# Performance work log

Measured on AMD Instinct MI355X. Metric: run time of the kernel, lower is better.

Reference implementation:

```python
import jax, jax.numpy as jnp
import numpy as np

NEG = 1e12


def _sincos(seq_len, dim):
    # SinusoidalPositionEmbedding with merge_mode='zero': [1, S, dim] interleaved (sin, cos)
    pos = jnp.arange(seq_len, dtype=jnp.float32)
    inv = jnp.power(10000.0, -2.0 * jnp.arange(dim // 2, dtype=jnp.float32) / dim)
    emb = pos[:, None] * inv[None, :]                      # [S, dim/2]
    emb = jnp.stack([jnp.sin(emb), jnp.cos(emb)], axis=-1).reshape(seq_len, dim)
    cos_pos = jnp.repeat(emb[:, 1::2], 2, axis=-1)[None]   # [1, S, dim]
    sin_pos = jnp.repeat(emb[:, ::2], 2, axis=-1)[None]    # [1, S, dim]
    return cos_pos, sin_pos


def _rope(x, cos_pos, sin_pos):
    # x: [B, S, d]; rotate pairs: (-x1, x0, -x3, x2, ...)
    x2 = jnp.stack([-x[..., 1::2], x[..., ::2]], axis=-1).reshape(x.shape)
    return x * cos_pos + x2 * sin_pos


def _pointer_head(hidden, mask_f, W1, b1, W2, b2, inner_dim):
    B, S, _ = hidden.shape
    out = hidden @ W1 + b1                                 # [B, S, 2*inner_dim]
    qw, kw = out[..., ::2], out[..., 1::2]                 # [B, S, inner_dim]
    cos_pos, sin_pos = _sincos(S, inner_dim)
    qw = _rope(qw, cos_pos, sin_pos)
    kw = _rope(kw, cos_pos, sin_pos)
    logits = jnp.einsum('bmd,bnd->bmn', qw, kw) / (inner_dim ** 0.5)  # [B, S, S]
    bias = jnp.transpose(hidden @ W2 + b2, (0, 2, 1)) / 2.0           # [B, 2T, S]
    # [B, T, S, S]
    logits = logits[:, None] + bias[:, ::2, None, :] + bias[:, 1::2, :, None]
    # sequence masking on key axis (last) and query axis (second-to-last)
    mk = mask_f[:, None, None, :]
    mq = mask_f[:, None, :, None]
    logits = logits * mq - NEG * (1.0 - mq)
    logits = logits * mk - NEG * (1.0 - mk)
    # strict lower-triangular mask over (m, n)
    tril = jnp.tril(jnp.ones((S, S), dtype=logits.dtype), k=-1)
    logits = logits - tril * NEG
    return logits


def setup_inputs() -> dict:
    key = jax.random.key(0)
    ks = jax.random.split(key, 10)
    B, S, H = 8, 512, 768
    inner_dim, ent_t, arg_t = 64, 12, 16
    s = 0.02
    return {
        'last_hidden_state': jax.random.normal(ks[0], (B, S, H), jnp.float32),
        'attention_mask': jnp.ones((B, S), jnp.int32),
        'W1': jax.random.normal(ks[1], (H, inner_dim * 2), jnp.float32) * s,
        'b1': jax.random.normal(ks[2], (inner_dim * 2,), jnp.float32) * s,
        'W2': jax.random.normal(ks[3], (H, ent_t * 2), jnp.float32) * s,
        'b2': jax.random.normal(ks[4], (ent_t * 2,), jnp.float32) * s,
        'Wa1': jax.random.normal(ks[5], (H, inner_dim * 2), jnp.float32) * s,
        'ba1': jax.random.normal(ks[6], (inner_dim * 2,), jnp.float32) * s,
        'Wa2': jax.random.normal(ks[7], (H, arg_t * 2), jnp.float32) * s,
        'ba2': jax.random.normal(ks[8], (arg_t * 2,), jnp.float32) * s,
    }


def reference(last_hidden_state, attention_mask, W1, b1, W2, b2, Wa1, ba1, Wa2, ba2):
    inner_dim = W1.shape[1] // 2
    mask_f = attention_mask.astype(last_hidden_state.dtype)
    logits = _pointer_head(last_hidden_state, mask_f, W1, b1, W2, b2, inner_dim)
    argument_logits = _pointer_head(last_hidden_state, mask_f, Wa1, ba1, Wa2, ba2, inner_dim)
    return logits, argument_logits
```

## Files before the change

### kernel.cpp

```cpp
#include <hip/hip_runtime.h>
#include <hip/hip_bf16.h>

typedef __attribute__((ext_vector_type(8))) short s16x8;
typedef __attribute__((ext_vector_type(4))) float f32x4;

#define NEGC 1000000000000.0f

constexpr int B_ = 8, S_ = 512, H_ = 768;
constexpr int ENT = 12, ARG = 16;
constexpr int NC = 320;
constexpr int ROWS = B_ * S_;
constexpr size_t OUT_ENT = (size_t)B_ * ENT * S_ * S_;

static __device__ __forceinline__ unsigned short f2bf(float x) {
  return __builtin_bit_cast(unsigned short, __float2bfloat16(x));
}

typedef const __attribute__((address_space(1))) unsigned int gu32;
typedef __attribute__((address_space(3))) unsigned int lu32;
static __device__ __forceinline__ void glds16(const void* g, void* l) {
  __builtin_amdgcn_global_load_lds((gu32*)g, (lu32*)l, 16, 0, 0);
}

__global__ __launch_bounds__(256) void k_prep(
    const float* __restrict__ X,
    const float* __restrict__ W1, const float* __restrict__ b1,
    const float* __restrict__ W2, const float* __restrict__ b2,
    const float* __restrict__ Wa1, const float* __restrict__ ba1,
    const float* __restrict__ Wa2, const float* __restrict__ ba2,
    __hip_bfloat16* __restrict__ Xb,
    __hip_bfloat16* __restrict__ Wt,
    float* __restrict__ bcat) {
  int idx = blockIdx.x * 256 + threadIdx.x;
  const int nx = ROWS * H_ / 4;
  if (idx < nx) {
    float4 v = reinterpret_cast<const float4*>(X)[idx];
    ushort4 o;
    o.x = f2bf(v.x); o.y = f2bf(v.y); o.z = f2bf(v.z); o.w = f2bf(v.w);
    reinterpret_cast<ushort4*>(Xb)[idx] = o;
    return;
  }
  idx -= nx;
  if (idx < NC * H_) {
    int n = idx / H_;
    int k = idx - n * H_;
    float v = 0.0f;
    if (n < 128)      v = W1[k * 128 + n];
    else if (n < 152) v = W2[k * 24 + (n - 128)];
    else if (n < 280) v = Wa1[k * 128 + (n - 152)];
    else if (n < 312) v = Wa2[k * 32 + (n - 280)];
    reinterpret_cast<unsigned short*>(Wt)[(size_t)n * H_ + k] = f2bf(v);
    return;
  }
  idx -= NC * H_;
  if (idx < NC) {
    int n = idx;
    float v = 0.0f;
    if (n < 128)      v = b1[n];
    else if (n < 152) v = b2[n - 128];
    else if (n < 280) v = ba1[n - 152];
    else if (n < 312) v = ba2[n - 280];
    bcat[n] = v;
  }
}

__global__ __launch_bounds__(256) void k_gemm(
    const __hip_bfloat16* __restrict__ Xb,
    const __hip_bfloat16* __restrict__ Wt,
    const float* __restrict__ bcat,
    __hip_bfloat16* __restrict__ qwe, __hip_bfloat16* __restrict__ kwe,
    __hip_bfloat16* __restrict__ qwa, __hip_bfloat16* __restrict__ kwa,
    float* __restrict__ kbe, float* __restrict__ qbe,
    float* __restrict__ kba, float* __restrict__ qba) {
  __shared__ __hip_bfloat16 XA[2][32 * 64];
  __shared__ __hip_bfloat16 WA[2][64 * 64];
  const int tid  = threadIdx.x;
  const int lane = tid & 63;
  const int w    = tid >> 6;
  const int wm   = w & 1;
  const int wn   = w >> 1;
  const int rl   = lane & 15;
  const int rg   = lane >> 4;
  const int row0 = blockIdx.y * 32;
  const int col0 = blockIdx.x * 64;
  const int lr = lane >> 3, cc = lane & 7;
  const int scs = cc ^ lr;

  const short* Xs = reinterpret_cast<const short*>(Xb);
  const short* Ws = reinterpret_cast<const short*>(Wt);
  const size_t xsrc  = (size_t)(row0 + w * 8 + lr) * H_ + scs * 8;
  const size_t wsrc0 = (size_t)(col0 + w * 16 + lr) * H_ + scs * 8;
  const size_t wsrc1 = (size_t)(col0 + w * 16 + 8 + lr) * H_ + scs * 8;

  auto stage = [&](int t, int buf) {
    const size_t ko = (size_t)t * 64;
    glds16(Xs + xsrc + ko,  &XA[buf][(w * 8) * 64]);
    glds16(Ws + wsrc0 + ko, &WA[buf][(w * 16) * 64]);
    glds16(Ws + wsrc1 + ko, &WA[buf][(w * 16 + 8) * 64]);
  };

  f32x4 acc[2] = {};
  auto compute = [&](int buf) {
    const short* xl = reinterpret_cast<const short*>(XA[buf]);
    const short* wl = reinterpret_cast<const short*>(WA[buf]);
#pragma unroll
    for (int ks = 0; ks < 2; ++ks) {
      const int gc = ks * 4 + rg;
      const int mloc = wm * 16 + rl;
      s16x8 bfrag = *reinterpret_cast<const s16x8*>(xl + mloc * 64 + (gc ^ (rl & 7)) * 8);
#pragma unroll
      for (int ni = 0; ni < 2; ++ni) {
        const int nloc = wn * 32 + ni * 16 + rl;
        s16x8 afrag = *reinterpret_cast<const s16x8*>(wl + nloc * 64 + (gc ^ (rl & 7)) * 8);
        acc[ni] = __builtin_amdgcn_mfma_f32_16x16x32_bf16(afrag, bfrag, acc[ni], 0, 0, 0);
      }
    }
  };

  stage(0, 0);
  asm volatile("s_waitcnt vmcnt(0)" ::: "memory");
  __syncthreads();
#pragma unroll 2
  for (int t = 0; t < 12; ++t) {
    if (t < 11) stage(t + 1, (t + 1) & 1);
    compute(t & 1);
    asm volatile("s_waitcnt vmcnt(0)" ::: "memory");
    __syncthreads();
  }

  const int r = row0 + wm * 16 + rl;
  const int b = r >> 9, mm = r & 511;
#pragma unroll
  for (int ni = 0; ni < 2; ++ni) {
    const int nq = col0 + wn * 32 + ni * 16 + rg * 4;
    if (nq >= 312) continue;
    float4 bc = *reinterpret_cast<const float4*>(bcat + nq);
    float v0 = acc[ni][0] + bc.x;
    float v1 = acc[ni][1] + bc.y;
    float v2 = acc[ni][2] + bc.z;
    float v3 = acc[ni][3] + bc.w;
    if (nq < 128 || (nq >= 152 && nq < 280)) {
      const bool ent = nq < 128;
      const int p = (ent ? nq : nq - 152) >> 2;
      float inv = exp2f(-(float)p * 0.4152410118609203f);
      float s, c;
      sincosf((float)mm * inv, &s, &c);
      unsigned int qpk = (unsigned int)f2bf(v0 * c - v2 * s) |
                         ((unsigned int)f2bf(v2 * c + v0 * s) << 16);
      unsigned int kpk = (unsigned int)f2bf(v1 * c - v3 * s) |
                         ((unsigned int)f2bf(v3 * c + v1 * s) << 16);
      short* qd = reinterpret_cast<short*>(ent ? qwe : qwa);
      short* kd = reinterpret_cast<short*>(ent ? kwe : kwa);
      *reinterpret_cast<unsigned int*>(qd + (size_t)r * 64 + 2 * p) = qpk;
      *reinterpret_cast<unsigned int*>(kd + (size_t)r * 64 + 2 * p) = kpk;
    } else {
      const bool ent = nq < 152;
      const int base = ent ? 128 : 280;
      const int T = ent ? ENT : ARG;
      float* qb = ent ? qbe : qba;
      float* kb = ent ? kbe : kba;
      float vv[4] = {v0, v1, v2, v3};
#pragma unroll
      for (int q = 0; q < 4; ++q) {
        int e = nq - base + q;
        int t = e >> 1;
        float* dst = (e & 1) ? qb : kb;
        dst[((size_t)b * T + t) * S_ + mm] = vv[q] * 0.5f;
      }
    }
  }
}

__global__ __launch_bounds__(256) void k_bcast(
    const __hip_bfloat16* __restrict__ qwe, const __hip_bfloat16* __restrict__ kwe,
    const __hip_bfloat16* __restrict__ qwa, const __hip_bfloat16* __restrict__ kwa,
    const float* __restrict__ kbe, const float* __restrict__ qbe,
    const float* __restrict__ kba, const float* __restrict__ qba,
    const int* __restrict__ mask,
    float* __restrict__ out) {
  const int lane = threadIdx.x & 63;
  const int w = threadIdx.x >> 6;
  const int hb = blockIdx.z;
  const int b = hb >> 1;
  const bool ent = (hb & 1) == 0;
  const int m0 = blockIdx.y * 64 + w * 16;
  const int n0 = blockIdx.x * 64;
  const int col = lane & 15;
  const int rg = lane >> 4;
  const int kseg = rg * 8;

  const short* qs = reinterpret_cast<const short*>(ent ? qwe : qwa);
  const short* ks = reinterpret_cast<const short*>(ent ? kwe : kwa);
  const float* qb = ent ? qbe : qba;
  const float* kb = ent ? kbe : kba;
  const int T = ent ? ENT : ARG;
  const size_t obase0 = ent ? (size_t)b * ENT * S_ * S_
                            : OUT_ENT + (size_t)b * ARG * S_ * S_;

  int mrow[4];
  float mqv[4], sqv[4];
#pragma unroll
  for (int j = 0; j < 4; ++j) {
    mrow[j] = m0 + rg * 4 + j;
    float mf = (float)mask[b * S_ + mrow[j]];
    mqv[j] = mf; sqv[j] = NEGC * (1.0f - mf);
  }
  int ncol[4];
  float mkv[4], skv[4];
#pragma unroll
  for (int f = 0; f < 4; ++f) {
    ncol[f] = n0 + 16 * f + col;
    float mf = (float)mask[b * S_ + ncol[f]];
    mkv[f] = mf; skv[f] = NEGC * (1.0f - mf);
  }
  float M[4][4], O[4][4];
#pragma unroll
  for (int f = 0; f < 4; ++f)
#pragma unroll
    for (int j = 0; j < 4; ++j) {
      M[f][j] = mqv[j] * mkv[f];
      O[f][j] = sqv[j] * mkv[f] + skv[f] + ((ncol[f] < mrow[j]) ? NEGC : 0.0f);
    }

  f32x4 acc[4] = {};
#pragma unroll
  for (int kk = 0; kk < 64; kk += 32) {
    s16x8 a = *reinterpret_cast<const s16x8*>(
        qs + (size_t)(b * S_ + m0 + col) * 64 + kk + kseg);
#pragma unroll
    for (int f = 0; f < 4; ++f) {
      s16x8 bb = *reinterpret_cast<const s16x8*>(
          ks + (size_t)(b * S_ + n0 + 16 * f + col) * 64 + kk + kseg);
      acc[f] = __builtin_amdgcn_mfma_f32_16x16x32_bf16(a, bb, acc[f], 0, 0, 0);
    }
  }
  float accMO[4][4];
#pragma unroll
  for (int f = 0; f < 4; ++f)
#pragma unroll
    for (int j = 0; j < 4; ++j)
      accMO[f][j] = acc[f][j] * 0.125f * M[f][j] - O[f][j];

  for (int t = 0; t < T; ++t) {
    const float* qbp = qb + ((size_t)b * T + t) * S_;
    const float* kbp = kb + ((size_t)b * T + t) * S_;
    float qv[4];
#pragma unroll
    for (int j = 0; j < 4; ++j) qv[j] = qbp[mrow[j]];
    size_t obase = obase0 + (size_t)t * S_ * S_;
#pragma unroll
    for (int f = 0; f < 4; ++f) {
      float kv = kbp[ncol[f]];
#pragma unroll
      for (int j = 0; j < 4; ++j) {
        float v = fmaf(kv + qv[j], M[f][j], accMO[f][j]);
        out[obase + (size_t)mrow[j] * S_ + ncol[f]] = v;
      }
    }
  }
}

extern "C" void kernel_launch(void* const* d_in, const int* in_sizes, int n_in,
                              void* d_out, int out_size, void* d_ws, size_t ws_size,
                              hipStream_t stream) {
  (void)in_sizes; (void)n_in; (void)out_size; (void)ws_size;
  const float* X   = (const float*)d_in[0];
  const int* mask  = (const int*)d_in[1];
  const float* W1  = (const float*)d_in[2];
  const float* b1  = (const float*)d_in[3];
  const float* W2  = (const float*)d_in[4];
  const float* b2  = (const float*)d_in[5];
  const float* Wa1 = (const float*)d_in[6];
  const float* ba1 = (const float*)d_in[7];
  const float* Wa2 = (const float*)d_in[8];
  const float* ba2 = (const float*)d_in[9];
  float* out = (float*)d_out;

  char* ws = (char*)d_ws;
  size_t off = 0;
  auto walloc = [&](size_t bytes) -> void* {
    void* p = ws + off;
    off += (bytes + 255) & ~(size_t)255;
    return p;
  };
  __hip_bfloat16* Xb  = (__hip_bfloat16*)walloc((size_t)ROWS * H_ * 2);
  __hip_bfloat16* Wt  = (__hip_bfloat16*)walloc((size_t)NC * H_ * 2);
  float* bcat         = (float*)walloc((size_t)NC * 4);
  __hip_bfloat16* qwe = (__hip_bfloat16*)walloc((size_t)ROWS * 64 * 2);
  __hip_bfloat16* kwe = (__hip_bfloat16*)walloc((size_t)ROWS * 64 * 2);
  __hip_bfloat16* qwa = (__hip_bfloat16*)walloc((size_t)ROWS * 64 * 2);
  __hip_bfloat16* kwa = (__hip_bfloat16*)walloc((size_t)ROWS * 64 * 2);
  float* kbe = (float*)walloc((size_t)B_ * ENT * S_ * 4);
  float* qbe = (float*)walloc((size_t)B_ * ENT * S_ * 4);
  float* kba = (float*)walloc((size_t)B_ * ARG * S_ * 4);
  float* qba = (float*)walloc((size_t)B_ * ARG * S_ * 4);

  const int prep_tasks = ROWS * H_ / 4 + NC * H_ + NC;
  k_prep<<<dim3((prep_tasks + 255) / 256), dim3(256), 0, stream>>>(
      X, W1, b1, W2, b2, Wa1, ba1, Wa2, ba2, Xb, Wt, bcat);
  k_gemm<<<dim3(5, 128), dim3(256), 0, stream>>>(
      Xb, Wt, bcat, qwe, kwe, qwa, kwa, kbe, qbe, kba, qba);
  k_bcast<<<dim3(8, 8, 16), dim3(256), 0, stream>>>(
      qwe, kwe, qwa, kwa, kbe, qbe, kba, qba, mask, out);
}
```

Measured before the change: 63.13 us.

## Split QK matmul from streaming broadcast kernel with vectorized row stores

Splits the fused kernel into a QK MFMA kernel that writes scaled scores to a bf16 workspace, plus a streaming kernel that adds the per-type biases and masks and writes each output row with 16-byte vector stores. The goal is better coalescing and parallelism for the large output write. In exchange it adds an extra launch and an intermediate buffer that is re-read once per type, and it rounds QK scores to bf16.

Result: slower. 68.45 us (+8.4%).

```diff
diff --git a/kernel.cpp b/kernel.cpp
--- a/kernel.cpp
+++ b/kernel.cpp
@@ -10,10 +10,14 @@
 constexpr int ENT = 12, ARG = 16;
 constexpr int NC = 320;
 constexpr int ROWS = B_ * S_;
-constexpr size_t OUT_ENT = (size_t)B_ * ENT * S_ * S_;
+constexpr size_t SS = (size_t)S_ * S_;
+constexpr size_t OUT_ENT = (size_t)B_ * ENT * SS;
 
 static __device__ __forceinline__ unsigned short f2bf(float x) {
   return __builtin_bit_cast(unsigned short, __float2bfloat16(x));
+}
+static __device__ __forceinline__ float bf2f(unsigned short u) {
+  return __builtin_bit_cast(float, (unsigned int)u << 16);
 }
 
 typedef const __attribute__((address_space(1))) unsigned int gu32;
@@ -171,13 +175,10 @@
   }
 }
 
-__global__ __launch_bounds__(256) void k_bcast(
+__global__ __launch_bounds__(256) void k_qk(
     const __hip_bfloat16* __restrict__ qwe, const __hip_bfloat16* __restrict__ kwe,
     const __hip_bfloat16* __restrict__ qwa, const __hip_bfloat16* __restrict__ kwa,
-    const float* __restrict__ kbe, const float* __restrict__ qbe,
-    const float* __restrict__ kba, const float* __restrict__ qba,
-    const int* __restrict__ mask,
-    float* __restrict__ out) {
+    unsigned short* __restrict__ qk) {
   const int lane = threadIdx.x & 63;
   const int w = threadIdx.x >> 6;
   const int hb = blockIdx.z;
@@ -185,78 +186,95 @@
   const bool ent = (hb & 1) == 0;
   const int m0 = blockIdx.y * 64 + w * 16;
   const int n0 = blockIdx.x * 64;
-  const int col = lane & 15;
+  const int cl = lane & 15;
   const int rg = lane >> 4;
   const int kseg = rg * 8;
 
   const short* qs = reinterpret_cast<const short*>(ent ? qwe : qwa);
   const short* ks = reinterpret_cast<const short*>(ent ? kwe : kwa);
-  const float* qb = ent ? qbe : qba;
-  const float* kb = ent ? kbe : kba;
+
+  f32x4 acc[4] = {};
+#pragma unroll
+  for (int kk = 0; kk < 64; kk += 32) {
+    s16x8 bq = *reinterpret_cast<const s16x8*>(
+        qs + (size_t)(b * S_ + m0 + cl) * 64 + kk + kseg);
+#pragma unroll
+    for (int f = 0; f < 4; ++f) {
+      s16x8 ak = *reinterpret_cast<const s16x8*>(
+          ks + (size_t)(b * S_ + n0 + f * 16 + cl) * 64 + kk + kseg);
+      acc[f] = __builtin_amdgcn_mfma_f32_16x16x32_bf16(ak, bq, acc[f], 0, 0, 0);
+    }
+  }
+  const size_t base = ((size_t)((ent ? 0 : 8) + b) * S_ + (m0 + cl)) * S_;
+#pragma unroll
+  for (int f = 0; f < 4; ++f) {
+    ushort4 o;
+    o.x = f2bf(acc[f][0] * 0.125f);
+    o.y = f2bf(acc[f][1] * 0.125f);
+    o.z = f2bf(acc[f][2] * 0.125f);
+    o.w = f2bf(acc[f][3] * 0.125f);
+    *reinterpret_cast<ushort4*>(qk + base + n0 + f * 16 + rg * 4) = o;
+  }
+}
+
+__global__ __launch_bounds__(256) void k_stream(
+    const unsigned short* __restrict__ qk,
+    const float* __restrict__ kbe, const float* __restrict__ qbe,
+    const float* __restrict__ kba, const float* __restrict__ qba,
+    const int* __restrict__ mask,
+    float* __restrict__ out) {
+  const int lane = threadIdx.x & 63;
+  const int w = threadIdx.x >> 6;
+  const int t = blockIdx.y;
+  const int b = blockIdx.z;
+  const bool ent = t < ENT;
+  const int tl = ent ? t : t - ENT;
   const int T = ent ? ENT : ARG;
-  const size_t obase0 = ent ? (size_t)b * ENT * S_ * S_
-                            : OUT_ENT + (size_t)b * ARG * S_ * S_;
-
-  int mrow[4];
-  float mqv[4], sqv[4];
-#pragma unroll
-  for (int j = 0; j < 4; ++j) {
-    mrow[j] = m0 + rg * 4 + j;
-    float mf = (float)mask[b * S_ + mrow[j]];
-    mqv[j] = mf; sqv[j] = NEGC * (1.0f - mf);
-  }
-  int ncol[4];
-  float mkv[4], skv[4];
-#pragma unroll
-  for (int f = 0; f < 4; ++f) {
-    ncol[f] = n0 + 16 * f + col;
-    float mf = (float)mask[b * S_ + ncol[f]];
-    mkv[f] = mf; skv[f] = NEGC * (1.0f - mf);
-  }
-  float M[4][4], O[4][4];
-#pragma unroll
-  for (int f = 0; f < 4; ++f)
-#pragma unroll
-    for (int j = 0; j < 4; ++j) {
-      M[f][j] = mqv[j] * mkv[f];
-      O[f][j] = sqv[j] * mkv[f] + skv[f] + ((ncol[f] < mrow[j]) ? NEGC : 0.0f);
+
+  const float* qbp = (ent ? qbe : qba) + ((size_t)b * T + tl) * S_;
+  const float* kbp = (ent ? kbe : kba) + ((size_t)b * T + tl) * S_;
+  const size_t qkbase = ((size_t)((ent ? 0 : 8) + b) * S_) * S_;
+  float* op = out + (ent ? ((size_t)b * ENT + tl) * SS
+                         : OUT_ENT + ((size_t)b * ARG + tl) * SS);
+
+  const int cA = lane * 4;
+  const int cB = 256 + lane * 4;
+
+  f32x4 kvA = *reinterpret_cast<const f32x4*>(kbp + cA);
+  f32x4 kvB = *reinterpret_cast<const f32x4*>(kbp + cB);
+  int4 miA = *reinterpret_cast<const int4*>(mask + b * S_ + cA);
+  int4 miB = *reinterpret_cast<const int4*>(mask + b * S_ + cB);
+  float mkA[4] = {(float)miA.x, (float)miA.y, (float)miA.z, (float)miA.w};
+  float mkB[4] = {(float)miB.x, (float)miB.y, (float)miB.z, (float)miB.w};
+  float skA[4], skB[4];
+#pragma unroll
+  for (int i = 0; i < 4; ++i) {
+    skA[i] = NEGC * (1.0f - mkA[i]);
+    skB[i] = NEGC * (1.0f - mkB[i]);
+  }
+
+  const int m0 = blockIdx.x * 64 + w * 16;
+  for (int rr = 0; rr < 16; ++rr) {
+    const int r = m0 + rr;
+    const float mqf = (float)mask[b * S_ + r];
+    const float sq = NEGC * (1.0f - mqf);
+    const float qv = qbp[r];
+    ushort4 ua = *reinterpret_cast<const ushort4*>(qk + qkbase + (size_t)r * S_ + cA);
+    ushort4 ub = *reinterpret_cast<const ushort4*>(qk + qkbase + (size_t)r * S_ + cB);
+    float qa[4] = {bf2f(ua.x), bf2f(ua.y), bf2f(ua.z), bf2f(ua.w)};
+    float qb4[4] = {bf2f(ub.x), bf2f(ub.y), bf2f(ub.z), bf2f(ub.w)};
+    f32x4 vA, vB;
+#pragma unroll
+    for (int i = 0; i < 4; ++i) {
+      float MA = mqf * mkA[i];
+      float OA = sq * mkA[i] + skA[i] + ((cA + i < r) ? NEGC : 0.0f);
+      vA[i] = fmaf(qa[i] + kvA[i] + qv, MA, -OA);
+      float MB = mqf * mkB[i];
+      float OB = sq * mkB[i] + skB[i] + ((cB + i < r) ? NEGC : 0.0f);
+      vB[i] = fmaf(qb4[i] + kvB[i] + qv, MB, -OB);
     }
-
-  f32x4 acc[4] = {};
-#pragma unroll
-  for (int kk = 0; kk < 64; kk += 32) {
-    s16x8 a = *reinterpret_cast<const s16x8*>(
-        qs + (size_t)(b * S_ + m0 + col) * 64 + kk + kseg);
-#pragma unroll
-    for (int f = 0; f < 4; ++f) {
-      s16x8 bb = *reinterpret_cast<const s16x8*>(
-          ks + (size_t)(b * S_ + n0 + 16 * f + col) * 64 + kk + kseg);
-      acc[f] = __builtin_amdgcn_mfma_f32_16x16x32_bf16(a, bb, acc[f], 0, 0, 0);
-    }
-  }
-  float accMO[4][4];
-#pragma unroll
-  for (int f = 0; f < 4; ++f)
-#pragma unroll
-    for (int j = 0; j < 4; ++j)
-      accMO[f][j] = acc[f][j] * 0.125f * M[f][j] - O[f][j];
-
-  for (int t = 0; t < T; ++t) {
-    const float* qbp = qb + ((size_t)b * T + t) * S_;
-    const float* kbp = kb + ((size_t)b * T + t) * S_;
-    float qv[4];
-#pragma unroll
-    for (int j = 0; j < 4; ++j) qv[j] = qbp[mrow[j]];
-    size_t obase = obase0 + (size_t)t * S_ * S_;
-#pragma unroll
-    for (int f = 0; f < 4; ++f) {
-      float kv = kbp[ncol[f]];
-#pragma unroll
-      for (int j = 0; j < 4; ++j) {
-        float v = fmaf(kv + qv[j], M[f][j], accMO[f][j]);
-        out[obase + (size_t)mrow[j] * S_ + ncol[f]] = v;
-      }
-    }
+    *reinterpret_cast<f32x4*>(op + (size_t)r * S_ + cA) = vA;
+    *reinterpret_cast<f32x4*>(op + (size_t)r * S_ + cB) = vB;
   }
 }
 
@@ -294,12 +312,14 @@
   float* qbe = (float*)walloc((size_t)B_ * ENT * S_ * 4);
   float* kba = (float*)walloc((size_t)B_ * ARG * S_ * 4);
   float* qba = (float*)walloc((size_t)B_ * ARG * S_ * 4);
+  unsigned short* qk = (unsigned short*)walloc((size_t)2 * B_ * SS * 2);
 
   const int prep_tasks = ROWS * H_ / 4 + NC * H_ + NC;
   k_prep<<<dim3((prep_tasks + 255) / 256), dim3(256), 0, stream>>>(
       X, W1, b1, W2, b2, Wa1, ba1, Wa2, ba2, Xb, Wt, bcat);
   k_gemm<<<dim3(5, 128), dim3(256), 0, stream>>>(
       Xb, Wt, bcat, qwe, kwe, qwa, kwa, kbe, qbe, kba, qba);
-  k_bcast<<<dim3(8, 8, 16), dim3(256), 0, stream>>>(
-      qwe, kwe, qwa, kwa, kbe, qbe, kba, qba, mask, out);
-}
+  k_qk<<<dim3(8, 8, 16), dim3(256), 0, stream>>>(qwe, kwe, qwa, kwa, qk);
+  k_stream<<<dim3(8, 28, 8), dim3(256), 0, stream>>>(
+      qk, kbe, qbe, kba, qba, mask, out);
+}
```
